# Optimization experiments

Measured on AMD Instinct MI355X. Metric: run time of the kernel, lower is better.

## Reference

```python
import jax, jax.numpy as jnp
import numpy as np
from jax import lax


def setup_inputs() -> dict:
    key = jax.random.key(0)
    ks = jax.random.split(key, 9)
    B, C, H, W = 32, 16, 128, 128
    x = jax.random.normal(ks[0], (B, C, H, W), dtype=jnp.float32)
    # sobel_x kernel as in source; the executed code leaves conv_sobel_x with tiled sobel_x.T
    sobel = jnp.array([[-1.0, 0.0, 1.0], [-2.0, 0.0, 2.0], [-1.0, 0.0, 1.0]], dtype=jnp.float32) / 8.0
    Wx = jnp.tile(sobel.T, (16, 16, 1, 1))  # [O=16, I=16, 3, 3]
    bx = jax.random.normal(ks[1], (16,), dtype=jnp.float32) * 0.05
    # conv_sobel_y retained its default (random) init in the source; model as random params
    Wy = jax.random.normal(ks[2], (16, 16, 3, 3), dtype=jnp.float32) * (1.0 / np.sqrt(16 * 9))
    by = jax.random.normal(ks[3], (16,), dtype=jnp.float32) * 0.05
    W1 = jax.random.normal(ks[4], (128, 48), dtype=jnp.float32) * (1.0 / np.sqrt(48))
    b1 = jax.random.normal(ks[5], (128,), dtype=jnp.float32) * 0.01
    W2 = jax.random.normal(ks[6], (16, 128), dtype=jnp.float32) * (1.0 / np.sqrt(128))
    b2 = jax.random.normal(ks[7], (16,), dtype=jnp.float32) * 0.01
    return {"x": x, "Wx": Wx, "bx": bx, "Wy": Wy, "by": by,
            "W1": W1, "b1": b1, "W2": W2, "b2": b2}


def _conv_same(x, w, b):
    # x: [B,C,H,W], w: [O,I,3,3] -> [B,O,H,W]
    y = lax.conv_general_dilated(x, w, window_strides=(1, 1), padding="SAME",
                                 dimension_numbers=("NCHW", "OIHW", "NCHW"))
    return y + b[None, :, None, None]


def reference(x, Wx, bx, Wy, by, W1, b1, W2, b2):
    # concat along channels: [B, 48, H, W]
    feat = jnp.concatenate([_conv_same(x, Wx, bx), _conv_same(x, Wy, by), x], axis=1)
    # torch transpose(1, 3): [B, W, H, 48]
    feat = jnp.transpose(feat, (0, 3, 2, 1))
    h = jax.nn.relu(jnp.einsum("bwhc,oc->bwho", feat, W1) + b1)
    out = jnp.einsum("bwhc,oc->bwho", h, W2) + b2  # [B, W, H, 16]
    return out
```

## Files before the change

kernel.cpp:

```cpp
#include <hip/hip_runtime.h>
#include <hip/hip_bf16.h>

typedef __hip_bfloat16 bf16;
typedef __attribute__((ext_vector_type(8))) short short8;
typedef __attribute__((ext_vector_type(4))) short short4v;
typedef __attribute__((ext_vector_type(4))) float float4v;

#define HALO_H 18
#define HALO_W 10
#define CS 24
#define KS 136
#define XS_W 6
#define XS_REG (XS_W * HALO_H * CS)
#define HS_EL (128 * KS)

#define W2B_EL 20480
#define WSF_BYTE 45056
#define XT_BYTE 65536

__device__ __forceinline__ unsigned int bfbits(float f) {
    bf16 h = __float2bfloat16(f);
    unsigned short u;
    __builtin_memcpy(&u, &h, 2);
    return (unsigned int)u;
}

__global__ void prep_all(const float* __restrict__ x,
                         const float* __restrict__ Wx, const float* __restrict__ bx,
                         const float* __restrict__ Wy, const float* __restrict__ by,
                         const float* __restrict__ W1, const float* __restrict__ b1,
                         const float* __restrict__ W2, const float* __restrict__ b2,
                         bf16* __restrict__ wsb, float* __restrict__ wsf,
                         bf16* __restrict__ xT, int tb) {
    int blk = blockIdx.x;
    int tid = threadIdx.x;
    if (blk < tb) {
        int b = blk >> 7;
        int w = tid >> 1, half = tid & 1;
        const float* src = x + (((size_t)(b * 16 + half * 8)) * 128 + (blk & 127)) * 128 + w;
        unsigned int pk[4];
#pragma unroll
        for (int i = 0; i < 4; ++i) {
            unsigned int lo = bfbits(src[(size_t)(2 * i) * 16384]);
            unsigned int hi = bfbits(src[(size_t)(2 * i + 1) * 16384]);
            pk[i] = lo | (hi << 16);
        }
        *(uint4*)(xT + ((size_t)blk * 128 + w) * 16 + half * 8) =
            make_uint4(pk[0], pk[1], pk[2], pk[3]);
        return;
    }
    int t = (blk - tb) * 256 + tid;
    int stride = 80 * 256;
    for (int f = t; f < 128 * 160; f += stride) {
        int j = f / 160, k = f - j * 160;
        int g = k >> 4, c = k & 15;
        float v = 0.0f;
        if (g < 9) {
            for (int o = 0; o < 16; ++o) {
                float wx = Wx[(o * 16 + c) * 9 + g];
                float wy = Wy[(o * 16 + c) * 9 + g];
                v = fmaf(W1[j * 48 + o], wx, v);
                v = fmaf(W1[j * 48 + 16 + o], wy, v);
            }
            if (g == 4) v += W1[j * 48 + 32 + c];
        }
        wsb[f] = __float2bfloat16(v);
    }
    for (int f = t; f < 2048; f += stride) wsb[W2B_EL + f] = __float2bfloat16(W2[f]);
    for (int j = t; j < 128; j += stride) {
        float v = b1[j];
        for (int o = 0; o < 16; ++o) {
            v = fmaf(W1[j * 48 + o], bx[o], v);
            v = fmaf(W1[j * 48 + 16 + o], by[o], v);
        }
        wsf[j] = v;
    }
    if (t < 16) wsf[128 + t] = b2[t];
}

__global__ __launch_bounds__(256, 2) void nca_mfma_t(const bf16* __restrict__ xT,
                                                     const bf16* __restrict__ wsb,
                                                     const float* __restrict__ wsf,
                                                     float* __restrict__ out,
                                                     int gridTiles) {
    __shared__ __align__(16) bf16 xs[2][XS_REG];
    __shared__ __align__(16) bf16 hs[2][HS_EL];

    const int tid = threadIdx.x;
    const int wave = tid >> 6;
    const int lane = tid & 63;
    const int hl = lane & 15;
    const int quad = lane >> 4;
    const int r0 = quad * 4;
    const int mgrp = wave >> 1;
    const int ngrp = wave & 1;

    short8 afrag[4][5];
#pragma unroll
    for (int mt = 0; mt < 4; ++mt) {
        int m = mgrp * 64 + mt * 16 + hl;
#pragma unroll
        for (int q = 0; q < 5; ++q)
            afrag[mt][q] = *(const short8*)(wsb + m * 160 + q * 32 + quad * 8);
    }
    short8 w2frag[4];
#pragma unroll
    for (int r = 0; r < 4; ++r)
        w2frag[r] = *(const short8*)(wsb + W2B_EL + hl * 128 + r * 32 + quad * 8);
    float b1r[4][4];
#pragma unroll
    for (int mt = 0; mt < 4; ++mt)
#pragma unroll
        for (int r = 0; r < 4; ++r) b1r[mt][r] = wsf[mgrp * 64 + mt * 16 + r0 + r];
    float b2r[4];
#pragma unroll
    for (int r = 0; r < 4; ++r) b2r[r] = wsf[128 + r0 + r];

    int sc_lds[4], sc_row[4], sc_col[4], sc_cf[4];
#pragma unroll
    for (int s = 0; s < 4; ++s) {
        int u = lane + 64 * s;
        int pos = u >> 1, cf = u & 1;
        int col = pos / HALO_H, row = pos - col * HALO_H;
        sc_lds[s] = ngrp * XS_REG + (col * HALO_H + row) * CS + cf * 8;
        sc_row[s] = row; sc_col[s] = col; sc_cf[s] = cf;
    }
    const bool has3 = (lane < 24);

    uint4 pre[4];
    bf16* xsf = (bf16*)xs;

#define LOAD_TILE(T)                                                                  \
    {                                                                                 \
        int b_ = (T) >> 7, rem_ = (T) & 127;                                          \
        int w0_ = (rem_ >> 3) * 8, h0_ = (rem_ & 7) * 16;                             \
        _Pragma("unroll")                                                             \
        for (int s = 0; s < 4; ++s) {                                                 \
            int gh = h0_ - 1 + sc_row[s];                                             \
            int gw = w0_ - 1 + ngrp * 4 + sc_col[s];                                  \
            bool ok = (s < 3 || has3) && ((unsigned)gh < 128u) && ((unsigned)gw < 128u); \
            long off = (((long)b_ << 14) + gh * 128 + gw) * 16 + (sc_cf[s] << 3);     \
            const uint4* p = (const uint4*)(xT + (ok ? off : 0));                     \
            uint4 v = *p;                                                             \
            if (!ok) { v.x = 0; v.y = 0; v.z = 0; v.w = 0; }                          \
            pre[s] = v;                                                               \
        }                                                                             \
    }

    int t = blockIdx.x;
    LOAD_TILE(t);
    int tb = 0;

    for (; t < 4096; t += gridTiles) {
        const int b = t >> 7;
        const int rem = t & 127;
        const int w0 = (rem >> 3) * 8;
        const int h0 = (rem & 7) * 16;

#pragma unroll
        for (int s = 0; s < 3; ++s)
            *(uint4*)(xsf + sc_lds[s]) = pre[s];
        if (has3) *(uint4*)(xsf + sc_lds[3]) = pre[3];

        int tn = t + gridTiles;
        if (tn < 4096) LOAD_TILE(tn);

        float4v acc[4][4];
#pragma unroll
        for (int mt = 0; mt < 4; ++mt)
#pragma unroll
            for (int nt = 0; nt < 4; ++nt) acc[mt][nt] = (float4v)0.0f;

        const bf16* xw = xsf + ngrp * XS_REG;
#pragma unroll
        for (int q = 0; q < 5; ++q) {
            int g = q * 2 + (quad >> 1);
            if (g > 8) g = 8;
            int kh = g / 3, kw = g - kh * 3;
            int c0 = (quad & 1) * 8;
            short8 bfrag[4];
#pragma unroll
            for (int nt = 0; nt < 4; ++nt)
                bfrag[nt] = *(const short8*)(xw + ((nt + kw) * HALO_H + hl + kh) * CS + c0);
#pragma unroll
            for (int nt = 0; nt < 4; ++nt)
#pragma unroll
                for (int mt = 0; mt < 4; ++mt)
                    acc[mt][nt] = __builtin_amdgcn_mfma_f32_16x16x32_bf16(
                        afrag[mt][q], bfrag[nt], acc[mt][nt], 0, 0, 0);
        }

        bf16* hsw = (bf16*)hs + tb * HS_EL;
#pragma unroll
        for (int mt = 0; mt < 4; ++mt)
#pragma unroll
            for (int nt = 0; nt < 4; ++nt) {
                int p = (ngrp * 4 + nt) * 16 + hl;
                int m = mgrp * 64 + mt * 16 + r0;
                short4v pk;
#pragma unroll
                for (int r = 0; r < 4; ++r) {
                    float v = acc[mt][nt][r] + b1r[mt][r];
                    v = fmaxf(v, 0.0f);
                    bf16 hb = __float2bfloat16(v);
                    pk[r] = *reinterpret_cast<short*>(&hb);
                }
                *(short4v*)(hsw + p * KS + m) = pk;
            }
        __syncthreads();

        float4v acc2[2];
        acc2[0] = (float4v)0.0f;
        acc2[1] = (float4v)0.0f;
#pragma unroll
        for (int r = 0; r < 4; ++r) {
#pragma unroll
            for (int i = 0; i < 2; ++i) {
                int p = (wave * 2 + i) * 16 + hl;
                short8 bfrag = *(const short8*)(hsw + p * KS + r * 32 + quad * 8);
                acc2[i] = __builtin_amdgcn_mfma_f32_16x16x32_bf16(
                    w2frag[r], bfrag, acc2[i], 0, 0, 0);
            }
        }

#pragma unroll
        for (int i = 0; i < 2; ++i) {
            int nt = wave * 2 + i;
            size_t ofs = (((size_t)b * 128 + (w0 + nt)) * 128 + (h0 + hl)) * 16 + r0;
            float4 v = make_float4(acc2[i][0] + b2r[0], acc2[i][1] + b2r[1],
                                   acc2[i][2] + b2r[2], acc2[i][3] + b2r[3]);
            *(float4*)(out + ofs) = v;
        }
        tb ^= 1;
    }
#undef LOAD_TILE
}

__global__ __launch_bounds__(256, 2) void nca_mfma_fb(const float* __restrict__ x,
                                                      const bf16* __restrict__ wsb,
                                                      const float* __restrict__ wsf,
                                                      float* __restrict__ out,
                                                      int gridTiles) {
    __shared__ bf16 xsb[HALO_W * HALO_H * CS];
    __shared__ bf16 hsb[128 * KS];

    const int tid = threadIdx.x;
    const int wave = tid >> 6;
    const int lane = tid & 63;
    const int hl = lane & 15;
    const int quad = lane >> 4;
    const int r0 = quad * 4;
    const int mgrp = wave >> 1;
    const int ngrp = wave & 1;

    short8 afrag[4][5];
#pragma unroll
    for (int mt = 0; mt < 4; ++mt) {
        int m = mgrp * 64 + mt * 16 + hl;
#pragma unroll
        for (int q = 0; q < 5; ++q)
            afrag[mt][q] = *(const short8*)(wsb + m * 160 + q * 32 + quad * 8);
    }
    short8 w2frag[4];
#pragma unroll
    for (int r = 0; r < 4; ++r)
        w2frag[r] = *(const short8*)(wsb + W2B_EL + hl * 128 + r * 32 + quad * 8);
    float b1r[4][4];
#pragma unroll
    for (int mt = 0; mt < 4; ++mt)
#pragma unroll
        for (int r = 0; r < 4; ++r) b1r[mt][r] = wsf[mgrp * 64 + mt * 16 + r0 + r];
    float b2r[4];
#pragma unroll
    for (int r = 0; r < 4; ++r) b2r[r] = wsf[128 + r0 + r];

    for (int t = blockIdx.x; t < 4096; t += gridTiles) {
        int b = t >> 7;
        int rem = t & 127;
        int wt = rem >> 3, ht = rem & 7;
        int h0 = ht * 16, w0 = wt * 8;

        __syncthreads();

        const float* xb = x + (size_t)b * 16 * 128 * 128;
        for (int f = tid; f < 16 * HALO_H * HALO_W; f += 256) {
            int c = f / (HALO_H * HALO_W);
            int rr = f - c * (HALO_H * HALO_W);
            int hh = rr / HALO_W;
            int ww = rr - hh * HALO_W;
            int gh = h0 - 1 + hh, gw = w0 - 1 + ww;
            float v = 0.0f;
            if ((unsigned)gh < 128u && (unsigned)gw < 128u)
                v = xb[(c * 128 + gh) * 128 + gw];
            xsb[(ww * HALO_H + hh) * CS + c] = __float2bfloat16(v);
        }
        __syncthreads();

        float4v acc[4][4];
#pragma unroll
        for (int mt = 0; mt < 4; ++mt)
#pragma unroll
            for (int nt = 0; nt < 4; ++nt) acc[mt][nt] = (float4v)0.0f;

#pragma unroll
        for (int q = 0; q < 5; ++q) {
            int g = q * 2 + (quad >> 1);
            if (g > 8) g = 8;
            int kh = g / 3, kw = g - kh * 3;
            int c0 = (quad & 1) * 8;
            short8 bfrag[4];
#pragma unroll
            for (int nt = 0; nt < 4; ++nt) {
                int ww = ngrp * 4 + nt + kw;
                bfrag[nt] = *(const short8*)(xsb + (ww * HALO_H + hl + kh) * CS + c0);
            }
#pragma unroll
            for (int nt = 0; nt < 4; ++nt)
#pragma unroll
                for (int mt = 0; mt < 4; ++mt)
                    acc[mt][nt] = __builtin_amdgcn_mfma_f32_16x16x32_bf16(
                        afrag[mt][q], bfrag[nt], acc[mt][nt], 0, 0, 0);
        }

#pragma unroll
        for (int mt = 0; mt < 4; ++mt)
#pragma unroll
            for (int nt = 0; nt < 4; ++nt) {
                int p = (ngrp * 4 + nt) * 16 + hl;
                int m = mgrp * 64 + mt * 16 + r0;
                short4v pk;
#pragma unroll
                for (int r = 0; r < 4; ++r) {
                    float v = acc[mt][nt][r] + b1r[mt][r];
                    v = fmaxf(v, 0.0f);
                    bf16 hb = __float2bfloat16(v);
                    pk[r] = *reinterpret_cast<short*>(&hb);
                }
                *(short4v*)(hsb + p * KS + m) = pk;
            }
        __syncthreads();

        float4v acc2[2];
        acc2[0] = (float4v)0.0f;
        acc2[1] = (float4v)0.0f;
#pragma unroll
        for (int r = 0; r < 4; ++r) {
#pragma unroll
            for (int i = 0; i < 2; ++i) {
                int p = (wave * 2 + i) * 16 + hl;
                short8 bfrag = *(const short8*)(hsb + p * KS + r * 32 + quad * 8);
                acc2[i] = __builtin_amdgcn_mfma_f32_16x16x32_bf16(
                    w2frag[r], bfrag, acc2[i], 0, 0, 0);
            }
        }

#pragma unroll
        for (int i = 0; i < 2; ++i) {
            int nt = wave * 2 + i;
            size_t ofs = (((size_t)b * 128 + (w0 + nt)) * 128 + (h0 + hl)) * 16 + r0;
            float4 v = make_float4(acc2[i][0] + b2r[0], acc2[i][1] + b2r[1],
                                   acc2[i][2] + b2r[2], acc2[i][3] + b2r[3]);
            *(float4*)(out + ofs) = v;
        }
    }
}

extern "C" void kernel_launch(void* const* d_in, const int* in_sizes, int n_in,
                              void* d_out, int out_size, void* d_ws, size_t ws_size,
                              hipStream_t stream) {
    const float* x  = (const float*)d_in[0];
    const float* Wx = (const float*)d_in[1];
    const float* bx = (const float*)d_in[2];
    const float* Wy = (const float*)d_in[3];
    const float* by = (const float*)d_in[4];
    const float* W1 = (const float*)d_in[5];
    const float* b1 = (const float*)d_in[6];
    const float* W2 = (const float*)d_in[7];
    const float* b2 = (const float*)d_in[8];
    bf16* wsb = (bf16*)d_ws;
    float* wsf = (float*)((char*)d_ws + WSF_BYTE);
    bf16* xT = (bf16*)((char*)d_ws + XT_BYTE);
    float* out = (float*)d_out;

    const size_t need = (size_t)XT_BYTE + (size_t)32 * 128 * 128 * 16 * 2;
    const bool big = ws_size >= need;
    const int tb = big ? 4096 : 0;

    hipLaunchKernelGGL(prep_all, dim3(tb + 80), dim3(256), 0, stream,
                       x, Wx, bx, Wy, by, W1, b1, W2, b2, wsb, wsf, xT, tb);
    if (big) {
        const int grid = 512;
        hipLaunchKernelGGL(nca_mfma_t, dim3(grid), dim3(256), 0, stream,
                           xT, wsb, wsf, out, grid);
    } else {
        const int grid = 1024;
        hipLaunchKernelGGL(nca_mfma_fb, dim3(grid), dim3(256), 0, stream,
                           x, wsb, wsf, out, grid);
    }
}
```

Baseline: 141.6 us.

## Halve tile width to four columns and split hidden units across waves for occupancy

Reworks the fused conv+MLP kernel to process 4-column by 16-row tiles instead of 8x16. Each wave now owns 32 hidden units over all 64 pixels rather than a 2x2 split. Per-thread accumulators and fragments shrink, shared memory drops to a single hidden buffer, launch bounds rise to 3 blocks per CU, and the grid doubles to 1024. The cost is an extra __syncthreads per tile after the LDS staging store, and halo reloads grow relative to useful work because the tiles are narrower.

```diff
diff --git a/kernel.cpp b/kernel.cpp
--- a/kernel.cpp
+++ b/kernel.cpp
@@ -7,16 +7,16 @@
 typedef __attribute__((ext_vector_type(4))) float float4v;
 
 #define HALO_H 18
-#define HALO_W 10
+#define HALO_W4 6
 #define CS 24
 #define KS 136
-#define XS_W 6
-#define XS_REG (XS_W * HALO_H * CS)
-#define HS_EL (128 * KS)
+#define XS_EL (HALO_W4 * HALO_H * CS)
 
 #define W2B_EL 20480
 #define WSF_BYTE 45056
 #define XT_BYTE 65536
+
+#define HALO_W 10
 
 __device__ __forceinline__ unsigned int bfbits(float f) {
     bf16 h = __float2bfloat16(f);
@@ -78,13 +78,13 @@
     if (t < 16) wsf[128 + t] = b2[t];
 }
 
-__global__ __launch_bounds__(256, 2) void nca_mfma_t(const bf16* __restrict__ xT,
-                                                     const bf16* __restrict__ wsb,
-                                                     const float* __restrict__ wsf,
-                                                     float* __restrict__ out,
-                                                     int gridTiles) {
-    __shared__ __align__(16) bf16 xs[2][XS_REG];
-    __shared__ __align__(16) bf16 hs[2][HS_EL];
+__global__ __launch_bounds__(256, 3) void nca_mfma_t4(const bf16* __restrict__ xT,
+                                                      const bf16* __restrict__ wsb,
+                                                      const float* __restrict__ wsf,
+                                                      float* __restrict__ out,
+                                                      int gridTiles) {
+    __shared__ __align__(16) bf16 xs[2][XS_EL];
+    __shared__ __align__(16) bf16 hs[64 * KS];
 
     const int tid = threadIdx.x;
     const int wave = tid >> 6;
@@ -92,13 +92,11 @@
     const int hl = lane & 15;
     const int quad = lane >> 4;
     const int r0 = quad * 4;
-    const int mgrp = wave >> 1;
-    const int ngrp = wave & 1;
-
-    short8 afrag[4][5];
-#pragma unroll
-    for (int mt = 0; mt < 4; ++mt) {
-        int m = mgrp * 64 + mt * 16 + hl;
+
+    short8 afrag[2][5];
+#pragma unroll
+    for (int mt = 0; mt < 2; ++mt) {
+        int m = wave * 32 + mt * 16 + hl;
 #pragma unroll
         for (int q = 0; q < 5; ++q)
             afrag[mt][q] = *(const short8*)(wsb + m * 160 + q * 32 + quad * 8);
@@ -107,71 +105,57 @@
 #pragma unroll
     for (int r = 0; r < 4; ++r)
         w2frag[r] = *(const short8*)(wsb + W2B_EL + hl * 128 + r * 32 + quad * 8);
-    float b1r[4][4];
-#pragma unroll
-    for (int mt = 0; mt < 4; ++mt)
-#pragma unroll
-        for (int r = 0; r < 4; ++r) b1r[mt][r] = wsf[mgrp * 64 + mt * 16 + r0 + r];
+    float b1r[2][4];
+#pragma unroll
+    for (int mt = 0; mt < 2; ++mt)
+#pragma unroll
+        for (int r = 0; r < 4; ++r) b1r[mt][r] = wsf[wave * 32 + mt * 16 + r0 + r];
     float b2r[4];
 #pragma unroll
     for (int r = 0; r < 4; ++r) b2r[r] = wsf[128 + r0 + r];
 
-    int sc_lds[4], sc_row[4], sc_col[4], sc_cf[4];
-#pragma unroll
-    for (int s = 0; s < 4; ++s) {
-        int u = lane + 64 * s;
-        int pos = u >> 1, cf = u & 1;
-        int col = pos / HALO_H, row = pos - col * HALO_H;
-        sc_lds[s] = ngrp * XS_REG + (col * HALO_H + row) * CS + cf * 8;
-        sc_row[s] = row; sc_col[s] = col; sc_cf[s] = cf;
-    }
-    const bool has3 = (lane < 24);
-
-    uint4 pre[4];
-    bf16* xsf = (bf16*)xs;
+    const bool hasu = (tid < 216);
+    const int pos = tid >> 1, scf = tid & 1;
+    const int scol = pos / HALO_H, srow = pos - scol * HALO_H;
+    const int slds = (scol * HALO_H + srow) * CS + scf * 8;
+
+    uint4 pre;
 
 #define LOAD_TILE(T)                                                                  \
     {                                                                                 \
-        int b_ = (T) >> 7, rem_ = (T) & 127;                                          \
-        int w0_ = (rem_ >> 3) * 8, h0_ = (rem_ & 7) * 16;                             \
-        _Pragma("unroll")                                                             \
-        for (int s = 0; s < 4; ++s) {                                                 \
-            int gh = h0_ - 1 + sc_row[s];                                             \
-            int gw = w0_ - 1 + ngrp * 4 + sc_col[s];                                  \
-            bool ok = (s < 3 || has3) && ((unsigned)gh < 128u) && ((unsigned)gw < 128u); \
-            long off = (((long)b_ << 14) + gh * 128 + gw) * 16 + (sc_cf[s] << 3);     \
-            const uint4* p = (const uint4*)(xT + (ok ? off : 0));                     \
-            uint4 v = *p;                                                             \
-            if (!ok) { v.x = 0; v.y = 0; v.z = 0; v.w = 0; }                          \
-            pre[s] = v;                                                               \
-        }                                                                             \
+        int b_ = (T) >> 8, rem_ = (T) & 255;                                          \
+        int w0_ = (rem_ >> 3) * 4, h0_ = (rem_ & 7) * 16;                             \
+        int gh = h0_ - 1 + srow, gw = w0_ - 1 + scol;                                 \
+        bool ok = hasu && ((unsigned)gh < 128u) && ((unsigned)gw < 128u);             \
+        long off = (((long)b_ << 14) + gh * 128 + gw) * 16 + (scf << 3);              \
+        const uint4* p = (const uint4*)(xT + (ok ? off : 0));                         \
+        uint4 v = *p;                                                                 \
+        if (!ok) { v.x = 0; v.y = 0; v.z = 0; v.w = 0; }                              \
+        pre = v;                                                                      \
     }
 
     int t = blockIdx.x;
     LOAD_TILE(t);
-    int tb = 0;
-
-    for (; t < 4096; t += gridTiles) {
-        const int b = t >> 7;
-        const int rem = t & 127;
-        const int w0 = (rem >> 3) * 8;
+    int buf = 0;
+
+    for (; t < 8192; t += gridTiles) {
+        const int b = t >> 8;
+        const int rem = t & 255;
+        const int w0 = (rem >> 3) * 4;
         const int h0 = (rem & 7) * 16;
 
-#pragma unroll
-        for (int s = 0; s < 3; ++s)
-            *(uint4*)(xsf + sc_lds[s]) = pre[s];
-        if (has3) *(uint4*)(xsf + sc_lds[3]) = pre[3];
+        if (hasu) *(uint4*)(&xs[buf][slds]) = pre;
+        __syncthreads();
 
         int tn = t + gridTiles;
-        if (tn < 4096) LOAD_TILE(tn);
-
-        float4v acc[4][4];
-#pragma unroll
-        for (int mt = 0; mt < 4; ++mt)
+        if (tn < 8192) LOAD_TILE(tn);
+
+        float4v acc[2][4];
+#pragma unroll
+        for (int mt = 0; mt < 2; ++mt)
 #pragma unroll
             for (int nt = 0; nt < 4; ++nt) acc[mt][nt] = (float4v)0.0f;
 
-        const bf16* xw = xsf + ngrp * XS_REG;
 #pragma unroll
         for (int q = 0; q < 5; ++q) {
             int g = q * 2 + (quad >> 1);
@@ -181,22 +165,21 @@
             short8 bfrag[4];
 #pragma unroll
             for (int nt = 0; nt < 4; ++nt)
-                bfrag[nt] = *(const short8*)(xw + ((nt + kw) * HALO_H + hl + kh) * CS + c0);
+                bfrag[nt] = *(const short8*)(&xs[buf][((nt + kw) * HALO_H + hl + kh) * CS + c0]);
 #pragma unroll
             for (int nt = 0; nt < 4; ++nt)
 #pragma unroll
-                for (int mt = 0; mt < 4; ++mt)
+                for (int mt = 0; mt < 2; ++mt)
                     acc[mt][nt] = __builtin_amdgcn_mfma_f32_16x16x32_bf16(
                         afrag[mt][q], bfrag[nt], acc[mt][nt], 0, 0, 0);
         }
 
-        bf16* hsw = (bf16*)hs + tb * HS_EL;
-#pragma unroll
-        for (int mt = 0; mt < 4; ++mt)
+#pragma unroll
+        for (int mt = 0; mt < 2; ++mt)
 #pragma unroll
             for (int nt = 0; nt < 4; ++nt) {
-                int p = (ngrp * 4 + nt) * 16 + hl;
-                int m = mgrp * 64 + mt * 16 + r0;
+                int p = nt * 16 + hl;
+                int m = wave * 32 + mt * 16 + r0;
                 short4v pk;
 #pragma unroll
                 for (int r = 0; r < 4; ++r) {
@@ -205,33 +188,21 @@
                     bf16 hb = __float2bfloat16(v);
                     pk[r] = *reinterpret_cast<short*>(&hb);
                 }
-                *(short4v*)(hsw + p * KS + m) = pk;
-            }
-        __syncthreads();
-
-        float4v acc2[2];
-        acc2[0] = (float4v)0.0f;
-        acc2[1] = (float4v)0.0f;
+                *(short4v*)(hs + p * KS + m) = pk;
+            }
+        __syncthreads();
+
+        float4v acc2 = (float4v)0.0f;
 #pragma unroll
         for (int r = 0; r < 4; ++r) {
-#pragma unroll
-            for (int i = 0; i < 2; ++i) {
-                int p = (wave * 2 + i) * 16 + hl;
-                short8 bfrag = *(const short8*)(hsw + p * KS + r * 32 + quad * 8);
-                acc2[i] = __builtin_amdgcn_mfma_f32_16x16x32_bf16(
-                    w2frag[r], bfrag, acc2[i], 0, 0, 0);
-            }
-        }
-
-#pragma unroll
-        for (int i = 0; i < 2; ++i) {
-            int nt = wave * 2 + i;
-            size_t ofs = (((size_t)b * 128 + (w0 + nt)) * 128 + (h0 + hl)) * 16 + r0;
-            float4 v = make_float4(acc2[i][0] + b2r[0], acc2[i][1] + b2r[1],
-                                   acc2[i][2] + b2r[2], acc2[i][3] + b2r[3]);
-            *(float4*)(out + ofs) = v;
-        }
-        tb ^= 1;
+            short8 bfrag = *(const short8*)(hs + (wave * 16 + hl) * KS + r * 32 + quad * 8);
+            acc2 = __builtin_amdgcn_mfma_f32_16x16x32_bf16(w2frag[r], bfrag, acc2, 0, 0, 0);
+        }
+
+        size_t ofs = (((size_t)b * 128 + (w0 + wave)) * 128 + (h0 + hl)) * 16 + r0;
+        *(float4*)(out + ofs) = make_float4(acc2[0] + b2r[0], acc2[1] + b2r[1],
+                                            acc2[2] + b2r[2], acc2[3] + b2r[3]);
+        buf ^= 1;
     }
 #undef LOAD_TILE
 }
@@ -389,8 +360,8 @@
     hipLaunchKernelGGL(prep_all, dim3(tb + 80), dim3(256), 0, stream,
                        x, Wx, bx, Wy, by, W1, b1, W2, b2, wsb, wsf, xT, tb);
     if (big) {
-        const int grid = 512;
-        hipLaunchKernelGGL(nca_mfma_t, dim3(grid), dim3(256), 0, stream,
+        const int grid = 1024;
+        hipLaunchKernelGGL(nca_mfma_t4, dim3(grid), dim3(256), 0, stream,
                            xT, wsb, wsf, out, grid);
     } else {
         const int grid = 1024;
```

Result: faster. 125.6 us (-11.4%).
